# Performance work log

Measured on AMD Instinct MI355X. Metric: run time of the kernel, lower is better.

The kernel has to match this reference:

```python
import jax, jax.numpy as jnp
import numpy as np

N = 262144          # nodes (divisible by 8 for 3 pooling stages)
E = 4194304         # edges (avg degree 16)
PAD = 6             # 2 extra edge slots per pooling stage
IN = 32
HID = (32, 32, 16)


def gcn_conv(x, W, b, src, dst, w):
    """PyG GCNConv: add self-loops, symmetric norm, x@W, scatter-add, +bias.
    src/dst: padded edge arrays; w: float mask (0 = inactive edge)."""
    n = x.shape[0]
    deg = jax.ops.segment_sum(w, dst, num_segments=n) + 1.0  # +1 self-loop
    dinv = jax.lax.rsqrt(deg)                                 # deg >= 1
    h = x @ W
    norm = dinv[src] * dinv[dst] * w                          # [E+PAD]
    out = jax.ops.segment_sum(norm[:, None] * h[src], dst, num_segments=n)
    out = out + (dinv * dinv)[:, None] * h                    # self-loop term
    return out + b


def graph_max_pool(x, src, dst, w, slot):
    """max over adjacent node pairs; keep edges with both endpoints < n//2;
    append edges (m-1,0) and (0,m-1) in pre-allocated padding slots."""
    n = x.shape[0]
    m = n // 2
    xp = jnp.max(x[: 2 * m].reshape(m, 2, x.shape[1]), axis=1)
    valid = ((src < m) & (dst < m)).astype(w.dtype)
    w = w * valid
    src = src.at[slot].set(m - 1).at[slot + 1].set(0)
    dst = dst.at[slot].set(0).at[slot + 1].set(m - 1)
    w = w.at[slot].set(1.0).at[slot + 1].set(1.0)
    return xp, src, dst, w


def setup_inputs() -> dict:
    key = jax.random.key(0)
    ks = jax.random.split(key, 8)
    x = jax.random.normal(ks[0], (N, IN), dtype=jnp.float32)
    edge_index = jax.random.randint(ks[1], (2, E), 0, N, dtype=jnp.int32)
    def lin(k, fi, fo):
        return jax.random.normal(k, (fi, fo), dtype=jnp.float32) / np.float32(np.sqrt(fi))
    return {
        "x": x,
        "edge_index": edge_index,
        "W1": lin(ks[2], IN, HID[0]), "b1": jnp.zeros((HID[0],), jnp.float32),
        "W2": lin(ks[3], HID[0], HID[1]), "b2": jnp.zeros((HID[1],), jnp.float32),
        "W3": lin(ks[4], HID[1], HID[2]), "b3": jnp.zeros((HID[2],), jnp.float32),
    }


def reference(x, edge_index, W1, b1, W2, b2, W3, b3):
    # fixed-size padded edge list with float validity mask
    src = jnp.concatenate([edge_index[0], jnp.zeros((PAD,), edge_index.dtype)])
    dst = jnp.concatenate([edge_index[1], jnp.zeros((PAD,), edge_index.dtype)])
    w = jnp.concatenate([jnp.ones((E,), jnp.float32), jnp.zeros((PAD,), jnp.float32)])

    h = jax.nn.relu(gcn_conv(x, W1, b1, src, dst, w))
    h, src, dst, w = graph_max_pool(h, src, dst, w, E)
    h = jax.nn.relu(gcn_conv(h, W2, b2, src, dst, w))
    h, src, dst, w = graph_max_pool(h, src, dst, w, E + 2)
    h = jax.nn.relu(gcn_conv(h, W3, b3, src, dst, w))
    latent, src, dst, w = graph_max_pool(h, src, dst, w, E + 4)
    return latent, jnp.stack([src, dst]), w
```

## Files before the change

### kernel.cpp

```cpp
#include <hip/hip_runtime.h>
#include <hip/hip_bf16.h>
#include <stdint.h>

#define N_NODES 262144
#define E_EDGES 4194304
#define SRC_OFF 524288
#define DST_OFF (524288 + 4194310)
#define W_OFF   (524288 + 2 * 4194310)
#define NSEG    64
#define SEG3    4608
#define SEG2X   13568
#define T3      (NSEG * SEG3)
#define T2X     (NSEG * SEG2X)
#define SCAT1_BLOCKS (E_EDGES * 16 / 256)
#define OUT_BLOCKS   (E_EDGES / 8 / 256)

using bf16 = __hip_bfloat16;
typedef float f4v __attribute__((ext_vector_type(4)));
typedef float f2v __attribute__((ext_vector_type(2)));

__device__ __forceinline__ float b2f(unsigned int u) {
    union { unsigned int i; float f; } v; v.i = u << 16; return v.f;
}

__device__ __forceinline__ void pk_atomic_add_raw(bf16* addr, uint32_t data) {
    asm volatile("global_atomic_pk_add_bf16 %0, %1, off" :: "v"(addr), "v"(data) : "memory");
}

__device__ __forceinline__ float dinv_of(const float* __restrict__ deg, int i, int n, int pads) {
    float extra = (pads && (i == 0 || i == n - 1)) ? 1.0f : 0.0f;
    return rsqrtf(deg[i] + 1.0f + extra);
}

__global__ void __launch_bounds__(256) prep_kernel(const int* __restrict__ ei,
        uint32_t* __restrict__ el3, int2* __restrict__ el2,
        uint32_t* __restrict__ cnt3, uint32_t* __restrict__ cnt2,
        float* __restrict__ deg1, float* __restrict__ deg2, float* __restrict__ deg3) {
    int t = blockIdx.x * 256 + threadIdx.x;
    int lane = threadIdx.x & 63;
    int seg = (t >> 6) & (NSEG - 1);
    int4 s0 = ((const int4*)ei)[2 * t];
    int4 s1 = ((const int4*)ei)[2 * t + 1];
    int4 d0 = ((const int4*)(ei + E_EDGES))[2 * t];
    int4 d1 = ((const int4*)(ei + E_EDGES))[2 * t + 1];

    atomicAdd(&deg1[d0.x], 1.0f); atomicAdd(&deg1[d0.y], 1.0f);
    atomicAdd(&deg1[d0.z], 1.0f); atomicAdd(&deg1[d0.w], 1.0f);
    atomicAdd(&deg1[d1.x], 1.0f); atomicAdd(&deg1[d1.y], 1.0f);
    atomicAdd(&deg1[d1.z], 1.0f); atomicAdd(&deg1[d1.w], 1.0f);

    int ss[8] = {s0.x, s0.y, s0.z, s0.w, s1.x, s1.y, s1.z, s1.w};
    int dd[8] = {d0.x, d0.y, d0.z, d0.w, d1.x, d1.y, d1.z, d1.w};
    int c3 = 0, c2 = 0;
#pragma unroll
    for (int j = 0; j < 8; ++j) {
        bool b3  = (ss[j] < 65536) & (dd[j] < 65536);
        bool b23 = (ss[j] < 131072) & (dd[j] < 131072);
        c3 += b3; c2 += (b23 & !b3);
    }
    int pk = c2 | (c3 << 16);
    pk += __shfl_xor(pk, 32); pk += __shfl_xor(pk, 16); pk += __shfl_xor(pk, 8);
    pk += __shfl_xor(pk, 4);  pk += __shfl_xor(pk, 2);  pk += __shfl_xor(pk, 1);
    uint32_t wt2 = (uint32_t)pk & 0xFFFFu, wt3 = (uint32_t)pk >> 16;
    uint32_t b3base = 0, b2base = 0;
    if (lane == 0) {
        b3base = atomicAdd(&cnt3[seg], wt3);
        b2base = atomicAdd(&cnt2[seg], wt2);
    }
    b3base = __shfl(b3base, 0, 64);
    b2base = __shfl(b2base, 0, 64);
    uint32_t r3 = b3base, r2 = b2base;
    uint64_t lt = (1ull << lane) - 1ull;
#pragma unroll
    for (int j = 0; j < 8; ++j) {
        int s = ss[j], d = dd[j];
        bool b3  = (s < 65536) & (d < 65536);
        bool b23 = (s < 131072) & (d < 131072);
        bool b2  = b23 & !b3;
        uint64_t m3 = __ballot(b3), m2 = __ballot(b2);
        if (b3) {
            uint32_t pos = r3 + (uint32_t)__popcll(m3 & lt);
            if (pos < SEG3) el3[seg * SEG3 + pos] = (uint32_t)s | ((uint32_t)d << 16);
            atomicAdd(&deg3[d], 1.0f);
        }
        if (b2) {
            uint32_t pos = r2 + (uint32_t)__popcll(m2 & lt);
            if (pos < SEG2X) el2[seg * SEG2X + pos] = make_int2(s, d);
        }
        if (b23) atomicAdd(&deg2[d], 1.0f);
        r3 += (uint32_t)__popcll(m3); r2 += (uint32_t)__popcll(m2);
    }
}

__global__ void __launch_bounds__(256) xform1_kernel(const float* __restrict__ xin,
        const float* __restrict__ W, const float* __restrict__ deg1,
        bf16* __restrict__ hs, bf16* __restrict__ agg) {
    constexpr int FIN = 32, FOUT = 32, NPB = 8;
    __shared__ float sW[FIN * FOUT];
    __shared__ float sx[NPB * FIN];
    int tid = threadIdx.x;
    for (int i = tid; i < FIN * FOUT; i += 256) sW[i] = W[i];
    int node0 = blockIdx.x * NPB;
    for (int i = tid; i < NPB * FIN; i += 256) sx[i] = xin[node0 * FIN + i];
    __syncthreads();
    int nl = tid / FOUT, j = tid % FOUT;
    int node = node0 + nl;
    float acc = 0.0f;
#pragma unroll
    for (int k = 0; k < FIN; ++k) acc += sx[nl * FIN + k] * sW[k * FOUT + j];
    bf16 v = __float2bfloat16(rsqrtf(deg1[node] + 1.0f) * acc);
    hs[node * FOUT + j]  = v;
    agg[node * FOUT + j] = v;
}

template <int FOUT>
__global__ void __launch_bounds__(256) xform_pool_kernel(const bf16* __restrict__ aggp,
        const float* __restrict__ degp, int prevN, int prevPads, const float* __restrict__ biasp,
        const float* __restrict__ W, const float* __restrict__ deg, int curN,
        bf16* __restrict__ hs, bf16* __restrict__ agg) {
    constexpr int FIN = 32;
    constexpr int NPB = 256 / FOUT;
    __shared__ float sW[FIN * FOUT];
    __shared__ float sx[NPB * FIN];
    const unsigned short* ap = (const unsigned short*)aggp;
    int tid = threadIdx.x;
    for (int i = tid; i < FIN * FOUT; i += 256) sW[i] = W[i];
    int node0 = blockIdx.x * NPB;
    for (int i = tid; i < NPB * FIN; i += 256) {
        int nl = i / FIN, k = i % FIN;
        int g0 = 2 * (node0 + nl);
        float bb = biasp[k];
        float v0 = dinv_of(degp, g0,     prevN, prevPads) * b2f(ap[(size_t)g0 * FIN + k])       + bb;
        float v1 = dinv_of(degp, g0 + 1, prevN, prevPads) * b2f(ap[(size_t)(g0 + 1) * FIN + k]) + bb;
        sx[i] = fmaxf(fmaxf(v0, v1), 0.0f);
    }
    __syncthreads();
    int nl = tid / FOUT, j = tid % FOUT;
    int node = node0 + nl;
    float acc = 0.0f;
#pragma unroll
    for (int k = 0; k < FIN; ++k) acc += sx[nl * FIN + k] * sW[k * FOUT + j];
    bf16 v = __float2bfloat16(dinv_of(deg, node, curN, 1) * acc);
    hs[node * FOUT + j]  = v;
    agg[node * FOUT + j] = v;
}

__global__ void __launch_bounds__(256) scatter1_kernel(const int* __restrict__ ei,
        const bf16* __restrict__ hs, bf16* __restrict__ agg, float* __restrict__ out) {
    if (blockIdx.x >= SCAT1_BLOCKS) {
        int t = (blockIdx.x - SCAT1_BLOCKS) * 256 + threadIdx.x;
        int4 s0 = ((const int4*)ei)[2 * t];
        int4 s1 = ((const int4*)ei)[2 * t + 1];
        int4 d0 = ((const int4*)(ei + E_EDGES))[2 * t];
        int4 d1 = ((const int4*)(ei + E_EDGES))[2 * t + 1];
        f4v v;
        v = (f4v){(float)s0.x, (float)s0.y, (float)s0.z, (float)s0.w};
        __builtin_nontemporal_store(v, (f4v*)(out + SRC_OFF) + 2 * t);
        v = (f4v){(float)s1.x, (float)s1.y, (float)s1.z, (float)s1.w};
        __builtin_nontemporal_store(v, (f4v*)(out + SRC_OFF) + 2 * t + 1);
        f2v w2;
        w2 = (f2v){(float)d0.x, (float)d0.y}; __builtin_nontemporal_store(w2, (f2v*)(out + DST_OFF) + 4 * t);
        w2 = (f2v){(float)d0.z, (float)d0.w}; __builtin_nontemporal_store(w2, (f2v*)(out + DST_OFF) + 4 * t + 1);
        w2 = (f2v){(float)d1.x, (float)d1.y}; __builtin_nontemporal_store(w2, (f2v*)(out + DST_OFF) + 4 * t + 2);
        w2 = (f2v){(float)d1.z, (float)d1.w}; __builtin_nontemporal_store(w2, (f2v*)(out + DST_OFF) + 4 * t + 3);
        v = (f4v){(s0.x < 32768 && d0.x < 32768) ? 1.0f : 0.0f,
                  (s0.y < 32768 && d0.y < 32768) ? 1.0f : 0.0f,
                  (s0.z < 32768 && d0.z < 32768) ? 1.0f : 0.0f,
                  (s0.w < 32768 && d0.w < 32768) ? 1.0f : 0.0f};
        __builtin_nontemporal_store(v, (f4v*)(out + W_OFF) + 2 * t);
        v = (f4v){(s1.x < 32768 && d1.x < 32768) ? 1.0f : 0.0f,
                  (s1.y < 32768 && d1.y < 32768) ? 1.0f : 0.0f,
                  (s1.z < 32768 && d1.z < 32768) ? 1.0f : 0.0f,
                  (s1.w < 32768 && d1.w < 32768) ? 1.0f : 0.0f};
        __builtin_nontemporal_store(v, (f4v*)(out + W_OFF) + 2 * t + 1);
        if (blockIdx.x == SCAT1_BLOCKS && threadIdx.x < 6) {
            int k = threadIdx.x;
            int stage = k >> 1, m = 131072 >> stage;
            int s, d;
            if ((k & 1) == 0) { s = m - 1; d = 0; } else { s = 0; d = m - 1; }
            int e = E_EDGES + k;
            out[SRC_OFF + e] = (float)s;
            out[DST_OFF + e] = (float)d;
            out[W_OFF + e]   = (stage == 2) ? 1.0f : 0.0f;
        }
        return;
    }
    unsigned idx = blockIdx.x * 256u + threadIdx.x;
    int e = (int)(idx >> 4), p = (int)(idx & 15u);
    int s = ei[e], d = ei[E_EDGES + e];
    uint32_t hw = *(const uint32_t*)((const unsigned short*)hs + (size_t)s * 32 + 2 * p);
    pk_atomic_add_raw(agg + (size_t)d * 32 + 2 * p, hw);
}

__global__ void __launch_bounds__(256) scatter2_kernel(const uint32_t* __restrict__ el3,
        const int2* __restrict__ el2, const uint32_t* __restrict__ cnt3,
        const uint32_t* __restrict__ cnt2, const bf16* __restrict__ hs,
        bf16* __restrict__ agg) {
    unsigned idx = blockIdx.x * 256u + threadIdx.x;
    unsigned e = idx >> 4; int p = (int)(idx & 15u);
    int s, d;
    if (e < T3) {
        unsigned seg = e / SEG3, loc = e - seg * SEG3;
        if (loc >= cnt3[seg]) return;
        uint32_t v = el3[e];
        s = (int)(v & 0xFFFFu); d = (int)(v >> 16);
    } else if (e < T3 + T2X) {
        unsigned e2 = e - T3, seg = e2 / SEG2X, loc = e2 - seg * SEG2X;
        if (loc >= cnt2[seg]) return;
        int2 sd = el2[e2]; s = sd.x; d = sd.y;
    } else if (e == T3 + T2X)     { s = 131071; d = 0; }
    else if (e == T3 + T2X + 1)   { s = 0; d = 131071; }
    else return;
    uint32_t hw = *(const uint32_t*)((const unsigned short*)hs + (size_t)s * 32 + 2 * p);
    pk_atomic_add_raw(agg + (size_t)d * 32 + 2 * p, hw);
}

__global__ void __launch_bounds__(256) scatter3_kernel(const uint32_t* __restrict__ el3,
        const uint32_t* __restrict__ cnt3, const bf16* __restrict__ hs,
        bf16* __restrict__ agg) {
    unsigned idx = blockIdx.x * 256u + threadIdx.x;
    unsigned e = idx >> 3; int p = (int)(idx & 7u);
    int s, d;
    if (e < T3) {
        unsigned seg = e / SEG3, loc = e - seg * SEG3;
        if (loc >= cnt3[seg]) return;
        uint32_t v = el3[e];
        s = (int)(v & 0xFFFFu); d = (int)(v >> 16);
    } else if (e == T3)     { s = 65535; d = 0; }
    else if (e == T3 + 1)   { s = 0; d = 65535; }
    else return;
    uint32_t hw = *(const uint32_t*)((const unsigned short*)hs + (size_t)s * 16 + 2 * p);
    pk_atomic_add_raw(agg + (size_t)d * 16 + 2 * p, hw);
}

__global__ void __launch_bounds__(256) pool_out_kernel(const bf16* __restrict__ agg,
        const float* __restrict__ deg3, const float* __restrict__ bias,
        float* __restrict__ outp) {
    unsigned idx = blockIdx.x * 256u + threadIdx.x;
    int i = (int)(idx >> 4), f = (int)(idx & 15);
    int g0 = 2 * i;
    float bb = bias[f];
    float v0 = dinv_of(deg3, g0,     65536, 1) * __bfloat162float(agg[(size_t)g0 * 16 + f])       + bb;
    float v1 = dinv_of(deg3, g0 + 1, 65536, 1) * __bfloat162float(agg[(size_t)(g0 + 1) * 16 + f]) + bb;
    outp[idx] = fmaxf(fmaxf(v0, v1), 0.0f);
}

extern "C" void kernel_launch(void* const* d_in, const int* in_sizes, int n_in,
                              void* d_out, int out_size, void* d_ws, size_t ws_size,
                              hipStream_t stream) {
    const float* x  = (const float*)d_in[0];
    const int*   ei = (const int*)d_in[1];
    const float* W1 = (const float*)d_in[2];
    const float* b1 = (const float*)d_in[3];
    const float* W2 = (const float*)d_in[4];
    const float* b2 = (const float*)d_in[5];
    const float* W3 = (const float*)d_in[6];
    const float* b3 = (const float*)d_in[7];
    float* out = (float*)d_out;

    char* ws = (char*)d_ws;
    bf16*     agg   = (bf16*)ws;
    bf16*     hs    = (bf16*)(ws + (16u << 20));
    uint32_t* el3   = (uint32_t*)(ws + (44u << 20));
    int2*     el2   = (int2*)(ws + (46u << 20));
    float*    deg1  = (float*)(ws + (55u << 20));
    float*    deg2  = (float*)(ws + (56u << 20));
    float*    deg3  = (float*)(ws + (56u << 20) + (512u << 10));
    uint32_t* cnt3  = (uint32_t*)(ws + (56u << 20) + (768u << 10));
    uint32_t* cnt2  = cnt3 + NSEG;

    hipMemsetAsync(deg1, 0, (1u << 20) + (768u << 10) + 512u, stream);

    prep_kernel<<<2048, 256, 0, stream>>>(ei, el3, el2, cnt3, cnt2, deg1, deg2, deg3);

    xform1_kernel<<<N_NODES / 8, 256, 0, stream>>>(x, W1, deg1, hs, agg);
    scatter1_kernel<<<SCAT1_BLOCKS + OUT_BLOCKS, 256, 0, stream>>>(ei, hs, agg, out);

    xform_pool_kernel<32><<<131072 / 8, 256, 0, stream>>>(agg, deg1, 262144, 0, b1,
                                                          W2, deg2, 131072, hs, agg);
    scatter2_kernel<<<(int)((((unsigned)(T3 + T2X + 2)) * 16 + 255) / 256), 256, 0, stream>>>(
        el3, el2, cnt3, cnt2, hs, agg);

    xform_pool_kernel<16><<<65536 / 16, 256, 0, stream>>>(agg, deg2, 131072, 1, b2,
                                                          W3, deg3, 65536, hs, agg);
    scatter3_kernel<<<(int)((((unsigned)(T3 + 2)) * 8 + 255) / 256), 256, 0, stream>>>(
        el3, cnt3, hs, agg);

    pool_out_kernel<<<32768 * 16 / 256, 256, 0, stream>>>(agg, deg3, b3, out);
}
```

Measured before the change: 688.2 us.

## Drop compacted edge lists; filter full edge list in later scatters

Removes the wave-level ballot compaction that built per-segment edge lists for the pooled stages. Stages 2 and 3 now scan the full original edge list and skip edges outside the pooled node range, and the deg2/deg3 histograms move into scatter1. The output edge and mask writes move from scatter1 into the prep kernel. The prep kernel becomes simpler, but stages 2 and 3 now launch threads for all 4M edges (16 and 8 per edge) where they previously covered only the compacted subsets, which greatly increases the thread count and index reads.

```diff
diff --git a/kernel.cpp b/kernel.cpp
--- a/kernel.cpp
+++ b/kernel.cpp
@@ -7,13 +7,6 @@
 #define SRC_OFF 524288
 #define DST_OFF (524288 + 4194310)
 #define W_OFF   (524288 + 2 * 4194310)
-#define NSEG    64
-#define SEG3    4608
-#define SEG2X   13568
-#define T3      (NSEG * SEG3)
-#define T2X     (NSEG * SEG2X)
-#define SCAT1_BLOCKS (E_EDGES * 16 / 256)
-#define OUT_BLOCKS   (E_EDGES / 8 / 256)
 
 using bf16 = __hip_bfloat16;
 typedef float f4v __attribute__((ext_vector_type(4)));
@@ -32,63 +25,49 @@
     return rsqrtf(deg[i] + 1.0f + extra);
 }
 
-__global__ void __launch_bounds__(256) prep_kernel(const int* __restrict__ ei,
-        uint32_t* __restrict__ el3, int2* __restrict__ el2,
-        uint32_t* __restrict__ cnt3, uint32_t* __restrict__ cnt2,
-        float* __restrict__ deg1, float* __restrict__ deg2, float* __restrict__ deg3) {
+__global__ void __launch_bounds__(256) hist_kernel(const int* __restrict__ ei,
+        float* __restrict__ out, float* __restrict__ deg1) {
     int t = blockIdx.x * 256 + threadIdx.x;
-    int lane = threadIdx.x & 63;
-    int seg = (t >> 6) & (NSEG - 1);
     int4 s0 = ((const int4*)ei)[2 * t];
     int4 s1 = ((const int4*)ei)[2 * t + 1];
     int4 d0 = ((const int4*)(ei + E_EDGES))[2 * t];
     int4 d1 = ((const int4*)(ei + E_EDGES))[2 * t + 1];
 
+    f4v v;
+    v = (f4v){(float)s0.x, (float)s0.y, (float)s0.z, (float)s0.w};
+    __builtin_nontemporal_store(v, (f4v*)(out + SRC_OFF) + 2 * t);
+    v = (f4v){(float)s1.x, (float)s1.y, (float)s1.z, (float)s1.w};
+    __builtin_nontemporal_store(v, (f4v*)(out + SRC_OFF) + 2 * t + 1);
+    f2v w2;
+    w2 = (f2v){(float)d0.x, (float)d0.y}; __builtin_nontemporal_store(w2, (f2v*)(out + DST_OFF) + 4 * t);
+    w2 = (f2v){(float)d0.z, (float)d0.w}; __builtin_nontemporal_store(w2, (f2v*)(out + DST_OFF) + 4 * t + 1);
+    w2 = (f2v){(float)d1.x, (float)d1.y}; __builtin_nontemporal_store(w2, (f2v*)(out + DST_OFF) + 4 * t + 2);
+    w2 = (f2v){(float)d1.z, (float)d1.w}; __builtin_nontemporal_store(w2, (f2v*)(out + DST_OFF) + 4 * t + 3);
+    v = (f4v){(s0.x < 32768 && d0.x < 32768) ? 1.0f : 0.0f,
+              (s0.y < 32768 && d0.y < 32768) ? 1.0f : 0.0f,
+              (s0.z < 32768 && d0.z < 32768) ? 1.0f : 0.0f,
+              (s0.w < 32768 && d0.w < 32768) ? 1.0f : 0.0f};
+    __builtin_nontemporal_store(v, (f4v*)(out + W_OFF) + 2 * t);
+    v = (f4v){(s1.x < 32768 && d1.x < 32768) ? 1.0f : 0.0f,
+              (s1.y < 32768 && d1.y < 32768) ? 1.0f : 0.0f,
+              (s1.z < 32768 && d1.z < 32768) ? 1.0f : 0.0f,
+              (s1.w < 32768 && d1.w < 32768) ? 1.0f : 0.0f};
+    __builtin_nontemporal_store(v, (f4v*)(out + W_OFF) + 2 * t + 1);
+
     atomicAdd(&deg1[d0.x], 1.0f); atomicAdd(&deg1[d0.y], 1.0f);
     atomicAdd(&deg1[d0.z], 1.0f); atomicAdd(&deg1[d0.w], 1.0f);
     atomicAdd(&deg1[d1.x], 1.0f); atomicAdd(&deg1[d1.y], 1.0f);
     atomicAdd(&deg1[d1.z], 1.0f); atomicAdd(&deg1[d1.w], 1.0f);
 
-    int ss[8] = {s0.x, s0.y, s0.z, s0.w, s1.x, s1.y, s1.z, s1.w};
-    int dd[8] = {d0.x, d0.y, d0.z, d0.w, d1.x, d1.y, d1.z, d1.w};
-    int c3 = 0, c2 = 0;
-#pragma unroll
-    for (int j = 0; j < 8; ++j) {
-        bool b3  = (ss[j] < 65536) & (dd[j] < 65536);
-        bool b23 = (ss[j] < 131072) & (dd[j] < 131072);
-        c3 += b3; c2 += (b23 & !b3);
-    }
-    int pk = c2 | (c3 << 16);
-    pk += __shfl_xor(pk, 32); pk += __shfl_xor(pk, 16); pk += __shfl_xor(pk, 8);
-    pk += __shfl_xor(pk, 4);  pk += __shfl_xor(pk, 2);  pk += __shfl_xor(pk, 1);
-    uint32_t wt2 = (uint32_t)pk & 0xFFFFu, wt3 = (uint32_t)pk >> 16;
-    uint32_t b3base = 0, b2base = 0;
-    if (lane == 0) {
-        b3base = atomicAdd(&cnt3[seg], wt3);
-        b2base = atomicAdd(&cnt2[seg], wt2);
-    }
-    b3base = __shfl(b3base, 0, 64);
-    b2base = __shfl(b2base, 0, 64);
-    uint32_t r3 = b3base, r2 = b2base;
-    uint64_t lt = (1ull << lane) - 1ull;
-#pragma unroll
-    for (int j = 0; j < 8; ++j) {
-        int s = ss[j], d = dd[j];
-        bool b3  = (s < 65536) & (d < 65536);
-        bool b23 = (s < 131072) & (d < 131072);
-        bool b2  = b23 & !b3;
-        uint64_t m3 = __ballot(b3), m2 = __ballot(b2);
-        if (b3) {
-            uint32_t pos = r3 + (uint32_t)__popcll(m3 & lt);
-            if (pos < SEG3) el3[seg * SEG3 + pos] = (uint32_t)s | ((uint32_t)d << 16);
-            atomicAdd(&deg3[d], 1.0f);
-        }
-        if (b2) {
-            uint32_t pos = r2 + (uint32_t)__popcll(m2 & lt);
-            if (pos < SEG2X) el2[seg * SEG2X + pos] = make_int2(s, d);
-        }
-        if (b23) atomicAdd(&deg2[d], 1.0f);
-        r3 += (uint32_t)__popcll(m3); r2 += (uint32_t)__popcll(m2);
+    if (blockIdx.x == 0 && threadIdx.x < 6) {
+        int k = threadIdx.x;
+        int stage = k >> 1, m = 131072 >> stage;
+        int s, d;
+        if ((k & 1) == 0) { s = m - 1; d = 0; } else { s = 0; d = m - 1; }
+        int e = E_EDGES + k;
+        out[SRC_OFF + e] = (float)s;
+        out[DST_OFF + e] = (float)d;
+        out[W_OFF + e]   = (stage == 2) ? 1.0f : 0.0f;
     }
 }
 
@@ -146,88 +125,46 @@
 }
 
 __global__ void __launch_bounds__(256) scatter1_kernel(const int* __restrict__ ei,
-        const bf16* __restrict__ hs, bf16* __restrict__ agg, float* __restrict__ out) {
-    if (blockIdx.x >= SCAT1_BLOCKS) {
-        int t = (blockIdx.x - SCAT1_BLOCKS) * 256 + threadIdx.x;
-        int4 s0 = ((const int4*)ei)[2 * t];
-        int4 s1 = ((const int4*)ei)[2 * t + 1];
-        int4 d0 = ((const int4*)(ei + E_EDGES))[2 * t];
-        int4 d1 = ((const int4*)(ei + E_EDGES))[2 * t + 1];
-        f4v v;
-        v = (f4v){(float)s0.x, (float)s0.y, (float)s0.z, (float)s0.w};
-        __builtin_nontemporal_store(v, (f4v*)(out + SRC_OFF) + 2 * t);
-        v = (f4v){(float)s1.x, (float)s1.y, (float)s1.z, (float)s1.w};
-        __builtin_nontemporal_store(v, (f4v*)(out + SRC_OFF) + 2 * t + 1);
-        f2v w2;
-        w2 = (f2v){(float)d0.x, (float)d0.y}; __builtin_nontemporal_store(w2, (f2v*)(out + DST_OFF) + 4 * t);
-        w2 = (f2v){(float)d0.z, (float)d0.w}; __builtin_nontemporal_store(w2, (f2v*)(out + DST_OFF) + 4 * t + 1);
-        w2 = (f2v){(float)d1.x, (float)d1.y}; __builtin_nontemporal_store(w2, (f2v*)(out + DST_OFF) + 4 * t + 2);
-        w2 = (f2v){(float)d1.z, (float)d1.w}; __builtin_nontemporal_store(w2, (f2v*)(out + DST_OFF) + 4 * t + 3);
-        v = (f4v){(s0.x < 32768 && d0.x < 32768) ? 1.0f : 0.0f,
-                  (s0.y < 32768 && d0.y < 32768) ? 1.0f : 0.0f,
-                  (s0.z < 32768 && d0.z < 32768) ? 1.0f : 0.0f,
-                  (s0.w < 32768 && d0.w < 32768) ? 1.0f : 0.0f};
-        __builtin_nontemporal_store(v, (f4v*)(out + W_OFF) + 2 * t);
-        v = (f4v){(s1.x < 32768 && d1.x < 32768) ? 1.0f : 0.0f,
-                  (s1.y < 32768 && d1.y < 32768) ? 1.0f : 0.0f,
-                  (s1.z < 32768 && d1.z < 32768) ? 1.0f : 0.0f,
-                  (s1.w < 32768 && d1.w < 32768) ? 1.0f : 0.0f};
-        __builtin_nontemporal_store(v, (f4v*)(out + W_OFF) + 2 * t + 1);
-        if (blockIdx.x == SCAT1_BLOCKS && threadIdx.x < 6) {
-            int k = threadIdx.x;
-            int stage = k >> 1, m = 131072 >> stage;
-            int s, d;
-            if ((k & 1) == 0) { s = m - 1; d = 0; } else { s = 0; d = m - 1; }
-            int e = E_EDGES + k;
-            out[SRC_OFF + e] = (float)s;
-            out[DST_OFF + e] = (float)d;
-            out[W_OFF + e]   = (stage == 2) ? 1.0f : 0.0f;
-        }
-        return;
-    }
+        const bf16* __restrict__ hs, bf16* __restrict__ agg,
+        float* __restrict__ deg2, float* __restrict__ deg3) {
     unsigned idx = blockIdx.x * 256u + threadIdx.x;
     int e = (int)(idx >> 4), p = (int)(idx & 15u);
     int s = ei[e], d = ei[E_EDGES + e];
+    if (p == 0 && s < 131072 && d < 131072) {
+        atomicAdd(&deg2[d], 1.0f);
+        if (s < 65536 && d < 65536) atomicAdd(&deg3[d], 1.0f);
+    }
     uint32_t hw = *(const uint32_t*)((const unsigned short*)hs + (size_t)s * 32 + 2 * p);
     pk_atomic_add_raw(agg + (size_t)d * 32 + 2 * p, hw);
 }
 
-__global__ void __launch_bounds__(256) scatter2_kernel(const uint32_t* __restrict__ el3,
-        const int2* __restrict__ el2, const uint32_t* __restrict__ cnt3,
-        const uint32_t* __restrict__ cnt2, const bf16* __restrict__ hs,
-        bf16* __restrict__ agg) {
+__global__ void __launch_bounds__(256) scatter2_kernel(const int* __restrict__ ei,
+        const bf16* __restrict__ hs, bf16* __restrict__ agg) {
     unsigned idx = blockIdx.x * 256u + threadIdx.x;
     unsigned e = idx >> 4; int p = (int)(idx & 15u);
     int s, d;
-    if (e < T3) {
-        unsigned seg = e / SEG3, loc = e - seg * SEG3;
-        if (loc >= cnt3[seg]) return;
-        uint32_t v = el3[e];
-        s = (int)(v & 0xFFFFu); d = (int)(v >> 16);
-    } else if (e < T3 + T2X) {
-        unsigned e2 = e - T3, seg = e2 / SEG2X, loc = e2 - seg * SEG2X;
-        if (loc >= cnt2[seg]) return;
-        int2 sd = el2[e2]; s = sd.x; d = sd.y;
-    } else if (e == T3 + T2X)     { s = 131071; d = 0; }
-    else if (e == T3 + T2X + 1)   { s = 0; d = 131071; }
+    if (e < E_EDGES) {
+        s = ei[e]; d = ei[E_EDGES + e];
+        if (s >= 131072 || d >= 131072) return;
+    }
+    else if (e == E_EDGES)     { s = 131071; d = 0; }
+    else if (e == E_EDGES + 1) { s = 0; d = 131071; }
     else return;
     uint32_t hw = *(const uint32_t*)((const unsigned short*)hs + (size_t)s * 32 + 2 * p);
     pk_atomic_add_raw(agg + (size_t)d * 32 + 2 * p, hw);
 }
 
-__global__ void __launch_bounds__(256) scatter3_kernel(const uint32_t* __restrict__ el3,
-        const uint32_t* __restrict__ cnt3, const bf16* __restrict__ hs,
-        bf16* __restrict__ agg) {
+__global__ void __launch_bounds__(256) scatter3_kernel(const int* __restrict__ ei,
+        const bf16* __restrict__ hs, bf16* __restrict__ agg) {
     unsigned idx = blockIdx.x * 256u + threadIdx.x;
     unsigned e = idx >> 3; int p = (int)(idx & 7u);
     int s, d;
-    if (e < T3) {
-        unsigned seg = e / SEG3, loc = e - seg * SEG3;
-        if (loc >= cnt3[seg]) return;
-        uint32_t v = el3[e];
-        s = (int)(v & 0xFFFFu); d = (int)(v >> 16);
-    } else if (e == T3)     { s = 65535; d = 0; }
-    else if (e == T3 + 1)   { s = 0; d = 65535; }
+    if (e < E_EDGES) {
+        s = ei[e]; d = ei[E_EDGES + e];
+        if (s >= 65536 || d >= 65536) return;
+    }
+    else if (e == E_EDGES)     { s = 65535; d = 0; }
+    else if (e == E_EDGES + 1) { s = 0; d = 65535; }
     else return;
     uint32_t hw = *(const uint32_t*)((const unsigned short*)hs + (size_t)s * 16 + 2 * p);
     pk_atomic_add_raw(agg + (size_t)d * 16 + 2 * p, hw);
@@ -259,32 +196,28 @@
     float* out = (float*)d_out;
 
     char* ws = (char*)d_ws;
-    bf16*     agg   = (bf16*)ws;
-    bf16*     hs    = (bf16*)(ws + (16u << 20));
-    uint32_t* el3   = (uint32_t*)(ws + (44u << 20));
-    int2*     el2   = (int2*)(ws + (46u << 20));
-    float*    deg1  = (float*)(ws + (55u << 20));
-    float*    deg2  = (float*)(ws + (56u << 20));
-    float*    deg3  = (float*)(ws + (56u << 20) + (512u << 10));
-    uint32_t* cnt3  = (uint32_t*)(ws + (56u << 20) + (768u << 10));
-    uint32_t* cnt2  = cnt3 + NSEG;
-
-    hipMemsetAsync(deg1, 0, (1u << 20) + (768u << 10) + 512u, stream);
-
-    prep_kernel<<<2048, 256, 0, stream>>>(ei, el3, el2, cnt3, cnt2, deg1, deg2, deg3);
+    bf16*  agg  = (bf16*)ws;
+    bf16*  hs   = (bf16*)(ws + (16u << 20));
+    float* deg1 = (float*)(ws + (55u << 20));
+    float* deg2 = (float*)(ws + (56u << 20));
+    float* deg3 = (float*)(ws + (56u << 20) + (512u << 10));
+
+    hipMemsetAsync(deg1, 0, (1u << 20) + (768u << 10), stream);
+
+    hist_kernel<<<2048, 256, 0, stream>>>(ei, out, deg1);
 
     xform1_kernel<<<N_NODES / 8, 256, 0, stream>>>(x, W1, deg1, hs, agg);
-    scatter1_kernel<<<SCAT1_BLOCKS + OUT_BLOCKS, 256, 0, stream>>>(ei, hs, agg, out);
+    scatter1_kernel<<<E_EDGES * 16 / 256, 256, 0, stream>>>(ei, hs, agg, deg2, deg3);
 
     xform_pool_kernel<32><<<131072 / 8, 256, 0, stream>>>(agg, deg1, 262144, 0, b1,
                                                           W2, deg2, 131072, hs, agg);
-    scatter2_kernel<<<(int)((((unsigned)(T3 + T2X + 2)) * 16 + 255) / 256), 256, 0, stream>>>(
-        el3, el2, cnt3, cnt2, hs, agg);
+    scatter2_kernel<<<(int)((((unsigned)E_EDGES + 2) * 16 + 255) / 256), 256, 0, stream>>>(
+        ei, hs, agg);
 
     xform_pool_kernel<16><<<65536 / 16, 256, 0, stream>>>(agg, deg2, 131072, 1, b2,
                                                           W3, deg3, 65536, hs, agg);
-    scatter3_kernel<<<(int)((((unsigned)(T3 + 2)) * 8 + 255) / 256), 256, 0, stream>>>(
-        el3, cnt3, hs, agg);
+    scatter3_kernel<<<(int)((((unsigned)E_EDGES + 2) * 8 + 255) / 256), 256, 0, stream>>>(
+        ei, hs, agg);
 
     pool_out_kernel<<<32768 * 16 / 256, 256, 0, stream>>>(agg, deg3, b3, out);
 }
```

Result: slower. 744.9 us (+8.2%).
